# Kernel tuning notes

Measured on AMD Instinct MI355X. Metric: run time of the kernel, lower is better.

The kernel has to match this reference:

```python
import jax, jax.numpy as jnp
import numpy as np

MAX_DISP = 64  # init kwarg max_disp; feature_similarity='correlation'


def setup_inputs() -> dict:
    key = jax.random.key(0)
    k1, k2 = jax.random.split(key)
    shape = (8, 160, 320, 128)  # (b, h, w, c)
    left = jax.random.normal(k1, shape, dtype=jnp.float32)
    right = jax.random.normal(k2, shape, dtype=jnp.float32)
    return {"left_feature": left, "right_feature": right}


def reference(left_feature, right_feature):
    # Faithful to CostVolume.__call__ with feature_similarity='correlation':
    # cost[b,h,j,i] = mean_c( left[b,h,j,c] * right[b,h,j-i,c] ) for j >= i, else 0.
    b, h, w, c = left_feature.shape
    widx = jnp.arange(w)  # (w,)
    slices = []
    for i in range(MAX_DISP):  # fixed hyperparameter unroll, not a data dim
        # roll brings right[..., j-i, :] to position j along width; wrapped
        # positions j < i are masked to zero (original leaves them at init 0).
        corr = jnp.mean(left_feature * jnp.roll(right_feature, i, axis=2), axis=3)  # (b,h,w)
        corr = jnp.where(widx >= i, corr, jnp.zeros((), corr.dtype))
        slices.append(corr)
    return jnp.stack(slices, axis=-1)  # (b, h, w, max_disp)
```

## Files before the change

kernel.cpp:

```cpp
#include <hip/hip_runtime.h>

#define W  320
#define TJ 64

typedef __attribute__((ext_vector_type(8))) short   short8;
typedef __attribute__((ext_vector_type(4))) float   floatx4;

__device__ __forceinline__ unsigned short f2bf(float f) {
    unsigned int u = __float_as_uint(f);
    u += 0x7FFFu + ((u >> 16) & 1u);
    return (unsigned short)(u >> 16);
}

__global__ __launch_bounds__(512, 6)
void cost_volume_kernel(const float* __restrict__ Lg,
                        const float* __restrict__ Rg,
                        float* __restrict__ out) {
    __shared__ unsigned short S[(64 + 128) * 128];

    const int jt  = blockIdx.x;
    const int bh  = blockIdx.y;
    const int j0  = jt * TJ;
    const int tid = threadIdx.x;

    const int lr    = tid >> 5;
    const int half  = tid & 1;
    const int chunk = (tid & 31) >> 1;
    const int cf    = (tid & 31) << 2;

    const float* Lbase = Lg + (size_t)(bh * W + j0) * 128;
    #pragma unroll
    for (int p = 0; p < 4; ++p) {
        const int row = p * 16 + lr;
        floatx4 v = *(const floatx4*)(Lbase + (size_t)row * 128 + cf);
        uint2 d;
        d.x = (unsigned)f2bf(v.x) | ((unsigned)f2bf(v.y) << 16);
        d.y = (unsigned)f2bf(v.z) | ((unsigned)f2bf(v.w) << 16);
        const int sw = chunk ^ (row & 15);
        *(uint2*)&S[row * 128 + (sw << 3) + half * 4] = d;
    }

    const float* Rrow0 = Rg + (size_t)(bh * W) * 128;
    #pragma unroll
    for (int p = 0; p < 8; ++p) {
        const int rr = p * 16 + lr;
        const int k  = j0 - 63 + rr;
        floatx4 v;
        v.x = 0.f; v.y = 0.f; v.z = 0.f; v.w = 0.f;
        if (k >= 0 && k < W) v = *(const floatx4*)(Rrow0 + (size_t)k * 128 + cf);
        uint2 d;
        d.x = (unsigned)f2bf(v.x) | ((unsigned)f2bf(v.y) << 16);
        d.y = (unsigned)f2bf(v.z) | ((unsigned)f2bf(v.w) << 16);
        const int sw = chunk ^ (rr & 15);
        *(uint2*)&S[(64 + rr) * 128 + (sw << 3) + half * 4] = d;
    }

    __syncthreads();

    const int wave = tid >> 6;
    const int lane = tid & 63;
    const int col  = lane & 15;
    const int quad = lane >> 4;
    const int mt   = wave >> 1;
    const int g    = wave & 1;
    const int m0   = mt * 16;
    const int ntb  = mt + g * 3;
    const int NT   = g ? 2 : 3;

    floatx4 acc[3];
    #pragma unroll
    for (int t = 0; t < 3; ++t) { acc[t].x = 0.f; acc[t].y = 0.f; acc[t].z = 0.f; acc[t].w = 0.f; }

    #pragma unroll
    for (int ks = 0; ks < 4; ++ks) {
        const int sc = (ks * 4 + quad) ^ col;
        const short8 af = *(const short8*)&S[(m0 + col) * 128 + (sc << 3)];
        #pragma unroll
        for (int t = 0; t < 3; ++t) {
            if (t < NT) {
                const int nrow = 64 + (ntb + t) * 16 + col;
                const short8 bf = *(const short8*)&S[nrow * 128 + (sc << 3)];
                acc[t] = __builtin_amdgcn_mfma_f32_16x16x32_bf16(af, bf, acc[t], 0, 0, 0);
            }
        }
    }

    float* obase = out + (size_t)(bh * W + j0) * 64;
    #pragma unroll
    for (int t = 0; t < 3; ++t) {
        if (t < NT) {
            const int n = (ntb + t) * 16 + col;
            #pragma unroll
            for (int r = 0; r < 4; ++r) {
                const int m = m0 + quad * 4 + r;
                const int i = m + 63 - n;
                if (i >= 0 && i < 64) {
                    obase[m * 64 + i] = acc[t][r] * 0.0078125f;
                }
            }
        }
    }
}

extern "C" void kernel_launch(void* const* d_in, const int* in_sizes, int n_in,
                              void* d_out, int out_size, void* d_ws, size_t ws_size,
                              hipStream_t stream) {
    const float* L = (const float*)d_in[0];
    const float* R = (const float*)d_in[1];
    float* out = (float*)d_out;
    dim3 grid(W / TJ, 8 * 160);
    cost_volume_kernel<<<grid, 512, 0, stream>>>(L, R, out);
}
```

Measured before the change: 430.2 us.

## Load left operand directly into MFMA registers and remap blocks across XCDs

The left feature tile is no longer staged through shared memory. Each lane now loads its A fragment straight from global memory and converts it to bf16 in registers, which shrinks LDS use to the right tile only and allows the occupancy hint to rise from 6 to 8. The grid is flattened to 1D and each block index is remapped so consecutive work items for the same row land on the same XCD, aiming for better L2 reuse of the overlapping right rows. The cost is direct global loads of the left data, each lane reading two 16-byte pieces per k-step, and more registers held for the A fragments.

```diff
diff --git a/kernel.cpp b/kernel.cpp
--- a/kernel.cpp
+++ b/kernel.cpp
@@ -6,56 +6,29 @@
 typedef __attribute__((ext_vector_type(8))) short   short8;
 typedef __attribute__((ext_vector_type(4))) float   floatx4;
 
-__device__ __forceinline__ unsigned short f2bf(float f) {
+__device__ __forceinline__ unsigned int f2bf(float f) {
     unsigned int u = __float_as_uint(f);
     u += 0x7FFFu + ((u >> 16) & 1u);
-    return (unsigned short)(u >> 16);
+    return u >> 16;
 }
 
-__global__ __launch_bounds__(512, 6)
+__global__ __launch_bounds__(512, 8)
 void cost_volume_kernel(const float* __restrict__ Lg,
                         const float* __restrict__ Rg,
                         float* __restrict__ out) {
-    __shared__ unsigned short S[(64 + 128) * 128];
+    __shared__ unsigned short S[128 * 128];
 
-    const int jt  = blockIdx.x;
-    const int bh  = blockIdx.y;
-    const int j0  = jt * TJ;
-    const int tid = threadIdx.x;
+    const int lin  = blockIdx.x;
+    const int work = (lin & 7) * 800 + (lin >> 3);
+    const int bh   = work / 5;
+    const int jt   = work - bh * 5;
+    const int j0   = jt * TJ;
+    const int tid  = threadIdx.x;
 
     const int lr    = tid >> 5;
     const int half  = tid & 1;
     const int chunk = (tid & 31) >> 1;
     const int cf    = (tid & 31) << 2;
-
-    const float* Lbase = Lg + (size_t)(bh * W + j0) * 128;
-    #pragma unroll
-    for (int p = 0; p < 4; ++p) {
-        const int row = p * 16 + lr;
-        floatx4 v = *(const floatx4*)(Lbase + (size_t)row * 128 + cf);
-        uint2 d;
-        d.x = (unsigned)f2bf(v.x) | ((unsigned)f2bf(v.y) << 16);
-        d.y = (unsigned)f2bf(v.z) | ((unsigned)f2bf(v.w) << 16);
-        const int sw = chunk ^ (row & 15);
-        *(uint2*)&S[row * 128 + (sw << 3) + half * 4] = d;
-    }
-
-    const float* Rrow0 = Rg + (size_t)(bh * W) * 128;
-    #pragma unroll
-    for (int p = 0; p < 8; ++p) {
-        const int rr = p * 16 + lr;
-        const int k  = j0 - 63 + rr;
-        floatx4 v;
-        v.x = 0.f; v.y = 0.f; v.z = 0.f; v.w = 0.f;
-        if (k >= 0 && k < W) v = *(const floatx4*)(Rrow0 + (size_t)k * 128 + cf);
-        uint2 d;
-        d.x = (unsigned)f2bf(v.x) | ((unsigned)f2bf(v.y) << 16);
-        d.y = (unsigned)f2bf(v.z) | ((unsigned)f2bf(v.w) << 16);
-        const int sw = chunk ^ (rr & 15);
-        *(uint2*)&S[(64 + rr) * 128 + (sw << 3) + half * 4] = d;
-    }
-
-    __syncthreads();
 
     const int wave = tid >> 6;
     const int lane = tid & 63;
@@ -67,6 +40,37 @@
     const int ntb  = mt + g * 3;
     const int NT   = g ? 2 : 3;
 
+    const float* Rrow0 = Rg + (size_t)(bh * W) * 128;
+    #pragma unroll
+    for (int p = 0; p < 8; ++p) {
+        const int rr = p * 16 + lr;
+        const int k  = j0 - 63 + rr;
+        floatx4 v;
+        v.x = 0.f; v.y = 0.f; v.z = 0.f; v.w = 0.f;
+        if (k >= 0 && k < W) v = *(const floatx4*)(Rrow0 + (size_t)k * 128 + cf);
+        uint2 d;
+        d.x = f2bf(v.x) | (f2bf(v.y) << 16);
+        d.y = f2bf(v.z) | (f2bf(v.w) << 16);
+        const int sw = chunk ^ (rr & 15);
+        *(uint2*)&S[rr * 128 + (sw << 3) + half * 4] = d;
+    }
+
+    const float* Arow = Lg + (size_t)(bh * W + j0 + m0 + col) * 128 + quad * 8;
+    short8 af[4];
+    #pragma unroll
+    for (int ks = 0; ks < 4; ++ks) {
+        floatx4 lo = *(const floatx4*)(Arow + ks * 32);
+        floatx4 hi = *(const floatx4*)(Arow + ks * 32 + 4);
+        short8 a;
+        a[0] = (short)f2bf(lo.x); a[1] = (short)f2bf(lo.y);
+        a[2] = (short)f2bf(lo.z); a[3] = (short)f2bf(lo.w);
+        a[4] = (short)f2bf(hi.x); a[5] = (short)f2bf(hi.y);
+        a[6] = (short)f2bf(hi.z); a[7] = (short)f2bf(hi.w);
+        af[ks] = a;
+    }
+
+    __syncthreads();
+
     floatx4 acc[3];
     #pragma unroll
     for (int t = 0; t < 3; ++t) { acc[t].x = 0.f; acc[t].y = 0.f; acc[t].z = 0.f; acc[t].w = 0.f; }
@@ -74,13 +78,12 @@
     #pragma unroll
     for (int ks = 0; ks < 4; ++ks) {
         const int sc = (ks * 4 + quad) ^ col;
-        const short8 af = *(const short8*)&S[(m0 + col) * 128 + (sc << 3)];
         #pragma unroll
         for (int t = 0; t < 3; ++t) {
             if (t < NT) {
-                const int nrow = 64 + (ntb + t) * 16 + col;
+                const int nrow = (ntb + t) * 16 + col;
                 const short8 bf = *(const short8*)&S[nrow * 128 + (sc << 3)];
-                acc[t] = __builtin_amdgcn_mfma_f32_16x16x32_bf16(af, bf, acc[t], 0, 0, 0);
+                acc[t] = __builtin_amdgcn_mfma_f32_16x16x32_bf16(af[ks], bf, acc[t], 0, 0, 0);
             }
         }
     }
@@ -108,6 +111,6 @@
     const float* L = (const float*)d_in[0];
     const float* R = (const float*)d_in[1];
     float* out = (float*)d_out;
-    dim3 grid(W / TJ, 8 * 160);
+    dim3 grid(8 * 160 * (W / TJ));
     cost_volume_kernel<<<grid, 512, 0, stream>>>(L, R, out);
 }
```

New measurement: 445.0 us. 3.4% more time.
